# Performance work log

Hardware: AMD Instinct MI355X
Metric: run time of the kernel (lower is better)

The kernel has to match this reference:

```python
import jax, jax.numpy as jnp
import numpy as np

MASK_VALUE = -1e30


def setup_inputs() -> dict:
    key = jax.random.key(0)
    ks = jax.random.split(key, 8)
    B, N, M, D = 64, 1024, 128, 256
    c = jax.random.normal(ks[0], (B, N, D), dtype=jnp.float32)
    q = jax.random.normal(ks[1], (B, M, D), dtype=jnp.float32)
    c_mask = jax.random.randint(ks[2], (B, N), 0, 2, dtype=jnp.int32)
    q_mask = jax.random.randint(ks[3], (B, M), 0, 2, dtype=jnp.int32)
    w0 = jax.random.normal(ks[4], (D, 1), dtype=jnp.float32) * 0.06  # glorot-ish scale
    w1 = jax.random.normal(ks[5], (D, 1), dtype=jnp.float32) * 0.06
    wm = jax.random.normal(ks[6], (D,), dtype=jnp.float32) * 0.06
    bias = jnp.zeros((M,), dtype=jnp.float32)
    return {"c": c, "q": q, "c_mask": c_mask, "q_mask": q_mask,
            "w0": w0, "w1": w1, "wm": wm, "bias": bias}


def reference(c, q, c_mask, q_mask, w0, w1, wm, bias):
    # Trilinear similarity S[b,i,j] = c.w0 + q.w1 + sum_d c*wm*q + bias[j]
    sub0 = jnp.einsum('bnd,do->bno', c, w0)              # (B,N,1)
    sub1 = jnp.einsum('bmd,do->bom', q, w1)              # (B,1,M)
    sub2 = jnp.einsum('bnd,d,bmd->bnm', c, wm, q)        # (B,N,M)
    S = sub0 + sub1 + sub2 + bias                        # bias broadcast over last axis
    qm = q_mask.astype(jnp.float32)[:, None, :]          # (B,1,M)
    cm = c_mask.astype(jnp.float32)[:, :, None]          # (B,N,1)
    S_ = jax.nn.softmax(S + MASK_VALUE * (1.0 - qm), axis=-1)   # row softmax over query
    S_T = jnp.swapaxes(jax.nn.softmax(S + MASK_VALUE * (1.0 - cm), axis=1), 1, 2)  # (B,M,N)
    c2q = jnp.matmul(S_, q)                              # (B,N,D)
    q2c = jnp.matmul(jnp.matmul(S_, S_T), c)             # (B,N,D)
    return jnp.concatenate([c, c2q, c * c2q, c * q2c], axis=-1)  # (B,N,4D)
```

## Files before the change

### kernel.cpp

```cpp
#include <hip/hip_runtime.h>
#include <cfloat>

#define BB 64
#define NN 1024
#define MM 128
#define DD 256
#define MASKV (-1e30f)

typedef __attribute__((ext_vector_type(8))) short bf16x8;
typedef __attribute__((ext_vector_type(16))) float f32x16;

__device__ __forceinline__ unsigned short f2bf(float x) {
  union { float f; unsigned int u; } v; v.f = x;
  unsigned int r = v.u + 0x7fffu + ((v.u >> 16) & 1u);
  return (unsigned short)(r >> 16);
}
__device__ __forceinline__ float bf2f(unsigned short h) {
  union { float f; unsigned int u; } v; v.u = ((unsigned int)h) << 16;
  return v.f;
}
__device__ __forceinline__ void split8(const float* xs, uint4* hv, uint4* lv) {
  unsigned hp[4], lp[4];
  #pragma unroll
  for (int p = 0; p < 4; p++) {
    unsigned short h0 = f2bf(xs[2 * p]), h1 = f2bf(xs[2 * p + 1]);
    unsigned short g0 = f2bf(xs[2 * p] - bf2f(h0));
    unsigned short g1 = f2bf(xs[2 * p + 1] - bf2f(h1));
    hp[p] = (unsigned)h0 | ((unsigned)h1 << 16);
    lp[p] = (unsigned)g0 | ((unsigned)g1 << 16);
  }
  *hv = make_uint4(hp[0], hp[1], hp[2], hp[3]);
  *lv = make_uint4(lp[0], lp[1], lp[2], lp[3]);
}
__device__ __forceinline__ bf16x8 u2b(uint4 u) {
  union { uint4 a; bf16x8 b; } x; x.a = u; return x.b;
}

__global__ __launch_bounds__(256) void k_dots(
    const float* __restrict__ c, const float* __restrict__ q,
    const int* __restrict__ qmask,
    const float* __restrict__ w0, const float* __restrict__ w1,
    const float* __restrict__ bias,
    float* __restrict__ sub0, float* __restrict__ qtermM) {
  int wave = (blockIdx.x * blockDim.x + threadIdx.x) >> 6;
  int lane = threadIdx.x & 63;
  const int total = BB * NN + BB * MM;
  if (wave >= total) return;
  const float* row;
  const float* w;
  if (wave < BB * NN) { row = c + (size_t)wave * DD; w = w0; }
  else                { row = q + (size_t)(wave - BB * NN) * DD; w = w1; }
  float4 v  = *(const float4*)(row + lane * 4);
  float4 wv = *(const float4*)(w   + lane * 4);
  float s = v.x * wv.x + v.y * wv.y + v.z * wv.z + v.w * wv.w;
  #pragma unroll
  for (int off = 32; off > 0; off >>= 1) s += __shfl_xor(s, off, 64);
  if (lane == 0) {
    if (wave < BB * NN) {
      sub0[wave] = s;
    } else {
      int r = wave - BB * NN;
      int m = r & (MM - 1);
      qtermM[r] = s + bias[m] + (qmask[r] ? 0.0f : MASKV);
    }
  }
}

__global__ __launch_bounds__(256) void k_zero(float* __restrict__ p) {
  p[blockIdx.x * 256 + threadIdx.x] = 0.0f;
}

__global__ __launch_bounds__(256) void k_pack_q(
    const float* __restrict__ q,
    unsigned short* __restrict__ dsth, unsigned short* __restrict__ dstl) {
  const int b = blockIdx.y;
  const int u = blockIdx.x * 4 + (threadIdx.x >> 6);
  const int f = u >> 3, ks = u & 7;
  const int l = threadIdx.x & 63;
  const int l31 = l & 31, lh = l >> 5;
  const float* sb = q + (size_t)b * MM * DD + (size_t)(ks * 16 + lh * 8) * DD + f * 32 + l31;
  float ys[8];
  #pragma unroll
  for (int j = 0; j < 8; j++) ys[j] = sb[(size_t)j * DD];
  uint4 hv, lv;
  split8(ys, &hv, &lv);
  size_t off = (size_t)b * 32768 + (size_t)(u * 64 + l) * 8;
  *(uint4*)(dsth + off) = hv;
  *(uint4*)(dstl + off) = lv;
}

__global__ __launch_bounds__(256) void k_pack_a(
    const float* __restrict__ Apart, const float* __restrict__ colsum,
    unsigned short* __restrict__ dsth, unsigned short* __restrict__ dstl) {
  const int b = blockIdx.y;
  const int u = blockIdx.x * 4 + (threadIdx.x >> 6);
  const int f = u >> 3, ks = u & 7;
  const int l = threadIdx.x & 63;
  const int l31 = l & 31, lh = l >> 5;
  const int m0 = ks * 16 + lh * 8;
  const size_t P = (size_t)BB * MM * DD;
  const float* sb = Apart + (size_t)b * MM * DD + (size_t)m0 * DD + f * 32 + l31;
  float ys[8];
  #pragma unroll
  for (int j = 0; j < 8; j++) {
    float v = sb[(size_t)j * DD] + sb[P + (size_t)j * DD] +
              sb[2 * P + (size_t)j * DD] + sb[3 * P + (size_t)j * DD];
    ys[j] = v * (1.0f / colsum[b * MM + m0 + j]);
  }
  uint4 hv, lv;
  split8(ys, &hv, &lv);
  size_t off = (size_t)b * 32768 + (size_t)(u * 64 + l) * 8;
  *(uint4*)(dsth + off) = hv;
  *(uint4*)(dstl + off) = lv;
}

__global__ __launch_bounds__(256) void k_score(
    const float* __restrict__ c, const float* __restrict__ q,
    const int* __restrict__ cmask, const float* __restrict__ wm,
    const float* __restrict__ sub0, const float* __restrict__ qtermM,
    unsigned short* __restrict__ Sfh, unsigned short* __restrict__ Sfl,
    unsigned short* __restrict__ EThi, unsigned short* __restrict__ ETlo,
    float* __restrict__ colsum) {
  __shared__ unsigned short smem[32768];
  unsigned short* cwh = smem;
  unsigned short* cwl = smem + 8192;
  unsigned short* qhi = smem + 16384;
  unsigned short* qlo = smem + 24576;
  const int b = blockIdx.y;
  const int n0 = blockIdx.x * 128;
  const int t = threadIdx.x;
  const int w = t >> 6;
  const int l = t & 63;
  const int l31 = l & 31;
  const int lh = l >> 5;

  f32x16 acc[4];
  #pragma unroll
  for (int mb = 0; mb < 4; mb++)
    #pragma unroll
    for (int i = 0; i < 16; i++) acc[mb][i] = 0.0f;

  for (int k0 = 0; k0 < DD; k0 += 64) {
    __syncthreads();
    #pragma unroll
    for (int g = 0; g < 4; g++) {
      int lin = t + g * 256;
      int row = lin >> 3;
      int kg  = (lin & 7) * 8;
      unsigned boff = (unsigned)(row * 128 + ((kg * 2) ^ ((row & 7) << 4)));
      float4 w0v = *(const float4*)(wm + k0 + kg);
      float4 w1v = *(const float4*)(wm + k0 + kg + 4);
      const float* cp = c + (size_t)(b * NN + n0 + row) * DD + k0 + kg;
      float4 a0 = *(const float4*)cp;
      float4 a1 = *(const float4*)(cp + 4);
      float xs[8] = {a0.x * w0v.x, a0.y * w0v.y, a0.z * w0v.z, a0.w * w0v.w,
                     a1.x * w1v.x, a1.y * w1v.y, a1.z * w1v.z, a1.w * w1v.w};
      uint4 hv, lv;
      split8(xs, &hv, &lv);
      *(uint4*)((char*)cwh + boff) = hv;
      *(uint4*)((char*)cwl + boff) = lv;
      const float* qp = q + (size_t)(b * MM + row) * DD + k0 + kg;
      float4 b0 = *(const float4*)qp;
      float4 b1 = *(const float4*)(qp + 4);
      float ys[8] = {b0.x, b0.y, b0.z, b0.w, b1.x, b1.y, b1.z, b1.w};
      split8(ys, &hv, &lv);
      *(uint4*)((char*)qhi + boff) = hv;
      *(uint4*)((char*)qlo + boff) = lv;
    }
    __syncthreads();
    #pragma unroll
    for (int ks = 0; ks < 64; ks += 16) {
      int ak = ks + lh * 8;
      unsigned arow = (unsigned)(w * 32 + l31);
      unsigned aoff = arow * 128 + (((unsigned)(ak * 2)) ^ ((arow & 7) << 4));
      bf16x8 ah = *(const bf16x8*)((const char*)cwh + aoff);
      bf16x8 al = *(const bf16x8*)((const char*)cwl + aoff);
      #pragma unroll
      for (int mb = 0; mb < 4; mb++) {
        unsigned brow = (unsigned)(mb * 32 + l31);
        unsigned boff2 = brow * 128 + (((unsigned)(ak * 2)) ^ ((brow & 7) << 4));
        bf16x8 bh = *(const bf16x8*)((const char*)qhi + boff2);
        bf16x8 bl = *(const bf16x8*)((const char*)qlo + boff2);
        acc[mb] = __builtin_amdgcn_mfma_f32_32x32x16_bf16(ah, bh, acc[mb], 0, 0, 0);
        acc[mb] = __builtin_amdgcn_mfma_f32_32x32x16_bf16(ah, bl, acc[mb], 0, 0, 0);
        acc[mb] = __builtin_amdgcn_mfma_f32_32x32x16_bf16(al, bh, acc[mb], 0, 0, 0);
      }
    }
  }

  unsigned* stile = (unsigned*)smem;
  unsigned short* eth = smem;
  unsigned short* etl = smem + 16384;
  __syncthreads();

  float qt[4];
  #pragma unroll
  for (int mb = 0; mb < 4; mb++) qt[mb] = qtermM[b * MM + mb * 32 + l31];

  float s0m[16];
  float ps[4] = {0.f, 0.f, 0.f, 0.f};
  #pragma unroll
  for (int g = 0; g < 4; g++) {
    #pragma unroll
    for (int j = 0; j < 4; j++) {
      int r = 4 * g + j;
      int row = j + 8 * g + 4 * lh;
      int gn = n0 + w * 32 + row;
      float sv = sub0[b * NN + gn] + (cmask[b * NN + gn] ? 0.0f : MASKV);
      s0m[g * 4 + j] = sv;
      float x[4];
      float vmax = -FLT_MAX;
      #pragma unroll
      for (int mb = 0; mb < 4; mb++) { x[mb] = acc[mb][r] + qt[mb]; vmax = fmaxf(vmax, x[mb]); }
      #pragma unroll
      for (int off = 16; off > 0; off >>= 1) vmax = fmaxf(vmax, __shfl_xor(vmax, off, 64));
      float e[4];
      float vsum = 0.0f;
      #pragma unroll
      for (int mb = 0; mb < 4; mb++) { e[mb] = __expf(x[mb] - vmax); vsum += e[mb]; }
      #pragma unroll
      for (int off = 16; off > 0; off >>= 1) vsum += __shfl_xor(vsum, off, 64);
      float inv = 1.0f / vsum;
      int nloc = w * 32 + 8 * g + 4 * lh + j;
      unsigned swn = (unsigned)((nloc & 15) << 4);
      #pragma unroll
      for (int mb = 0; mb < 4; mb++) {
        float s = e[mb] * inv;
        unsigned short h = f2bf(s);
        unsigned short lo2 = f2bf(s - bf2f(h));
        unsigned v = (unsigned)h | ((unsigned)lo2 << 16);
        int m = mb * 32 + l31;
        *(unsigned*)((char*)stile + nloc * 512 + (((unsigned)(m * 4)) ^ swn)) = v;
        float Ev = __expf(acc[mb][r] + sv);
        ps[mb] += Ev;
      }
    }
  }
  #pragma unroll
  for (int mb = 0; mb < 4; mb++) {
    ps[mb] += __shfl_xor(ps[mb], 32, 64);
    if (lh == 0) atomicAdd(&colsum[b * MM + mb * 32 + l31], ps[mb]);
  }
  __syncthreads();

  {
    size_t tb = ((size_t)b * 32 + (size_t)blockIdx.x * 4 + w) * 4096;
    int nloc = w * 32 + l31;
    unsigned basen = (unsigned)(nloc * 512);
    unsigned swn = (unsigned)((nloc & 15) << 4);
    #pragma unroll
    for (int ks = 0; ks < 8; ks++) {
      unsigned mB = (unsigned)((lh * 8 + ks * 16) * 4);
      uint4 va = *(const uint4*)((const char*)stile + basen + (mB ^ swn));
      uint4 vb = *(const uint4*)((const char*)stile + basen + ((mB + 16) ^ swn));
      uint4 hv = make_uint4((va.x & 0xFFFFu) | (va.y << 16), (va.z & 0xFFFFu) | (va.w << 16),
                            (vb.x & 0xFFFFu) | (vb.y << 16), (vb.z & 0xFFFFu) | (vb.w << 16));
      uint4 lv = make_uint4((va.x >> 16) | (va.y & 0xFFFF0000u), (va.z >> 16) | (va.w & 0xFFFF0000u),
                            (vb.x >> 16) | (vb.y & 0xFFFF0000u), (vb.z >> 16) | (vb.w & 0xFFFF0000u));
      size_t off = tb + (size_t)(ks * 64 + l) * 8;
      *(uint4*)(Sfh + off) = hv;
      *(uint4*)(Sfl + off) = lv;
    }
  }
  __syncthreads();

  #pragma unroll
  for (int g = 0; g < 4; g++) {
    float evg[4][4];
    #pragma unroll
    for (int j = 0; j < 4; j++) {
      int r = 4 * g + j;
      #pragma unroll
      for (int mb = 0; mb < 4; mb++)
        evg[mb][j] = __expf(acc[mb][r] + s0m[g * 4 + j]);
    }
    int nloc = w * 32 + 8 * g + 4 * lh;
    #pragma unroll
    for (int mb = 0; mb < 4; mb++) {
      int m = mb * 32 + l31;
      unsigned short h[4], lo[4];
      #pragma unroll
      for (int j = 0; j < 4; j++) {
        h[j] = f2bf(evg[mb][j]);
        lo[j] = f2bf(evg[mb][j] - bf2f(h[j]));
      }
      unsigned addr = (unsigned)(m * 256 + ((nloc * 2) ^ ((m & 15) << 4)));
      *(uint2*)((char*)eth + addr) = make_uint2(
          (unsigned)h[0] | ((unsigned)h[1] << 16),
          (unsigned)h[2] | ((unsigned)h[3] << 16));
      *(uint2*)((char*)etl + addr) = make_uint2(
          (unsigned)lo[0] | ((unsigned)lo[1] << 16),
          (unsigned)lo[2] | ((unsigned)lo[3] << 16));
    }
  }
  __syncthreads();

  {
    int chunk = t & 15;
    int mrow0 = t >> 4;
    #pragma unroll
    for (int it = 0; it < 8; it++) {
      int m = it * 16 + mrow0;
      int sw = (chunk * 16) ^ ((m & 15) << 4);
      uint4 vh = *(const uint4*)((const char*)eth + m * 256 + sw);
      uint4 vl = *(const uint4*)((const char*)etl + m * 256 + sw);
      size_t gb = (size_t)(b * MM + m) * NN + n0 + chunk * 8;
      *(uint4*)(EThi + gb) = vh;
      *(uint4*)(ETlo + gb) = vl;
    }
  }
}

__global__ __launch_bounds__(512) void k_colA(
    const unsigned short* __restrict__ EThi, const unsigned short* __restrict__ ETlo,
    const float* __restrict__ c, float* __restrict__ Apart) {
  const int p = blockIdx.x;
  const int b = blockIdx.y;
  const int t = threadIdx.x;
  const int w = t >> 6;
  const int l = t & 63;
  const int l31 = l & 31, lh = l >> 5;
  const int d = w * 32 + l31;

  f32x16 acc[4];
  #pragma unroll
  for (int mf = 0; mf < 4; mf++)
    #pragma unroll
    for (int i = 0; i < 16; i++) acc[mf][i] = 0.0f;

  const float* cb = c + (size_t)b * NN * DD + d;
  const size_t etb = (size_t)b * MM * NN + (size_t)p * 256 + lh * 8;

  for (int ks = 0; ks < 16; ks++) {
    int nb = p * 256 + ks * 16 + lh * 8;
    float ys[8];
    #pragma unroll
    for (int j = 0; j < 8; j++) ys[j] = cb[(size_t)(nb + j) * DD];
    uint4 hv, lv;
    split8(ys, &hv, &lv);
    bf16x8 ah = u2b(hv), al = u2b(lv);
    #pragma unroll
    for (int mf = 0; mf < 4; mf++) {
      size_t eoff = etb + (size_t)(mf * 32 + l31) * NN + ks * 16;
      bf16x8 bh = *(const bf16x8*)(EThi + eoff);
      bf16x8 bl = *(const bf16x8*)(ETlo + eoff);
      acc[mf] = __builtin_amdgcn_mfma_f32_32x32x16_bf16(ah, bh, acc[mf], 0, 0, 0);
      acc[mf] = __builtin_amdgcn_mfma_f32_32x32x16_bf16(ah, bl, acc[mf], 0, 0, 0);
      acc[mf] = __builtin_amdgcn_mfma_f32_32x32x16_bf16(al, bh, acc[mf], 0, 0, 0);
    }
  }

  float* ap = Apart + (size_t)p * (BB * MM * DD);
  #pragma unroll
  for (int mf = 0; mf < 4; mf++) {
    size_t rowb = (size_t)(b * MM + mf * 32 + l31) * DD + w * 32 + 4 * lh;
    #pragma unroll
    for (int g = 0; g < 4; g++) {
      float4 o = make_float4(acc[mf][4 * g + 0], acc[mf][4 * g + 1],
                             acc[mf][4 * g + 2], acc[mf][4 * g + 3]);
      *(float4*)(ap + rowb + 8 * g) = o;
    }
  }
}

__global__ __launch_bounds__(512, 4) void k_out(
    const float* __restrict__ c,
    const unsigned short* __restrict__ Sfh, const unsigned short* __restrict__ Sfl,
    const unsigned short* __restrict__ qfh, const unsigned short* __restrict__ qfl,
    const unsigned short* __restrict__ afh, const unsigned short* __restrict__ afl,
    float* __restrict__ out) {
  const int b = blockIdx.y;
  const int n0 = blockIdx.x * 32;
  const int t = threadIdx.x;
  const int w = t >> 6;
  const int l = t & 63;
  const int l31 = l & 31;
  const int lh = l >> 5;

  f32x16 acc0, acc1;
  #pragma unroll
  for (int i = 0; i < 16; i++) { acc0[i] = 0.0f; acc1[i] = 0.0f; }

  const size_t so = ((size_t)b * 32 + blockIdx.x) * 4096 + (size_t)l * 8;
  const size_t fo = (size_t)b * 32768 + (size_t)(w * 8 * 64 + l) * 8;

  #pragma unroll
  for (int ks = 0; ks < 8; ks++) {
    bf16x8 ah = *(const bf16x8*)(Sfh + so + ks * 512);
    bf16x8 al = *(const bf16x8*)(Sfl + so + ks * 512);
    size_t off = fo + (size_t)(ks * 64) * 8;
    bf16x8 qh = *(const bf16x8*)(qfh + off);
    bf16x8 ql = *(const bf16x8*)(qfl + off);
    bf16x8 vh = *(const bf16x8*)(afh + off);
    bf16x8 vl = *(const bf16x8*)(afl + off);
    acc0 = __builtin_amdgcn_mfma_f32_32x32x16_bf16(ah, qh, acc0, 0, 0, 0);
    acc0 = __builtin_amdgcn_mfma_f32_32x32x16_bf16(ah, ql, acc0, 0, 0, 0);
    acc0 = __builtin_amdgcn_mfma_f32_32x32x16_bf16(al, qh, acc0, 0, 0, 0);
    acc1 = __builtin_amdgcn_mfma_f32_32x32x16_bf16(ah, vh, acc1, 0, 0, 0);
    acc1 = __builtin_amdgcn_mfma_f32_32x32x16_bf16(ah, vl, acc1, 0, 0, 0);
    acc1 = __builtin_amdgcn_mfma_f32_32x32x16_bf16(al, vh, acc1, 0, 0, 0);
  }

  const int d = w * 32 + l31;
  #pragma unroll
  for (int r = 0; r < 16; r++) {
    int row = (r & 3) + 8 * (r >> 2) + 4 * lh;
    int gn = n0 + row;
    float cv = c[(size_t)(b * NN + gn) * DD + d];
    size_t ob = (size_t)(b * NN + gn) * (4 * DD) + d;
    float v1 = acc0[r], v3 = acc1[r];
    out[ob]          = cv;
    out[ob + DD]     = v1;
    out[ob + 2 * DD] = cv * v1;
    out[ob + 3 * DD] = cv * v3;
  }
}

extern "C" void kernel_launch(void* const* d_in, const int* in_sizes, int n_in,
                              void* d_out, int out_size, void* d_ws, size_t ws_size,
                              hipStream_t stream) {
  const float* c     = (const float*)d_in[0];
  const float* q     = (const float*)d_in[1];
  const int*   cmask = (const int*)d_in[2];
  const int*   qmask = (const int*)d_in[3];
  const float* w0    = (const float*)d_in[4];
  const float* w1    = (const float*)d_in[5];
  const float* wm    = (const float*)d_in[6];
  const float* bias  = (const float*)d_in[7];
  float* out = (float*)d_out;
  float* ws  = (float*)d_ws;

  unsigned short* Sfh  = (unsigned short*)ws;
  unsigned short* Sfl  = Sfh + 8388608;
  unsigned short* EThi = (unsigned short*)(ws + 8388608);
  unsigned short* ETlo = (unsigned short*)(ws + 12582912);
  float* Apart  = ws + 16777216;
  unsigned short* qfh = (unsigned short*)(ws + 25165824);
  unsigned short* qfl = (unsigned short*)(ws + 26214400);
  unsigned short* afh = (unsigned short*)(ws + 27262976);
  unsigned short* afl = (unsigned short*)(ws + 28311552);
  float* sub0   = ws + 29360128;
  float* qtermM = ws + 29425664;
  float* colsum = ws + 29433856;

  k_dots<<<18432, 256, 0, stream>>>(c, q, qmask, w0, w1, bias, sub0, qtermM);
  k_zero<<<32, 256, 0, stream>>>(colsum);
  k_pack_q<<<dim3(16, BB), 256, 0, stream>>>(q, qfh, qfl);
  k_score<<<dim3(8, BB), 256, 0, stream>>>(c, q, cmask, wm, sub0, qtermM, Sfh, Sfl, EThi, ETlo, colsum);
  k_colA<<<dim3(4, BB), 512, 0, stream>>>(EThi, ETlo, c, Apart);
  k_pack_a<<<dim3(16, BB), 256, 0, stream>>>(Apart, colsum, afh, afl);
  k_out<<<dim3(32, BB), 512, 0, stream>>>(c, Sfh, Sfl, qfh, qfl, afh, afl, out);
}
```

Before: 487.7 us.

## Fuse row dot products into score kernel and split colA over more partitions

Removes the separate k_dots and k_zero kernels. The c·w0 and q·w1 dot products are now computed inside k_score's tile-load loop, reduced with shuffles and staged through shared memory. Colsum zeroing moves into k_pack_q. k_colA now splits N into 8 partitions instead of 4, which doubles the grid for more parallelism, and k_pack_a sums 8 partial buffers in exchange. The cost is a larger Apart workspace, more partial-sum traffic, and redundant q·w1 work in each score block.

```diff
diff --git a/kernel.cpp b/kernel.cpp
--- a/kernel.cpp
+++ b/kernel.cpp
@@ -36,44 +36,12 @@
   union { uint4 a; bf16x8 b; } x; x.a = u; return x.b;
 }
 
-__global__ __launch_bounds__(256) void k_dots(
-    const float* __restrict__ c, const float* __restrict__ q,
-    const int* __restrict__ qmask,
-    const float* __restrict__ w0, const float* __restrict__ w1,
-    const float* __restrict__ bias,
-    float* __restrict__ sub0, float* __restrict__ qtermM) {
-  int wave = (blockIdx.x * blockDim.x + threadIdx.x) >> 6;
-  int lane = threadIdx.x & 63;
-  const int total = BB * NN + BB * MM;
-  if (wave >= total) return;
-  const float* row;
-  const float* w;
-  if (wave < BB * NN) { row = c + (size_t)wave * DD; w = w0; }
-  else                { row = q + (size_t)(wave - BB * NN) * DD; w = w1; }
-  float4 v  = *(const float4*)(row + lane * 4);
-  float4 wv = *(const float4*)(w   + lane * 4);
-  float s = v.x * wv.x + v.y * wv.y + v.z * wv.z + v.w * wv.w;
-  #pragma unroll
-  for (int off = 32; off > 0; off >>= 1) s += __shfl_xor(s, off, 64);
-  if (lane == 0) {
-    if (wave < BB * NN) {
-      sub0[wave] = s;
-    } else {
-      int r = wave - BB * NN;
-      int m = r & (MM - 1);
-      qtermM[r] = s + bias[m] + (qmask[r] ? 0.0f : MASKV);
-    }
-  }
-}
-
-__global__ __launch_bounds__(256) void k_zero(float* __restrict__ p) {
-  p[blockIdx.x * 256 + threadIdx.x] = 0.0f;
-}
-
 __global__ __launch_bounds__(256) void k_pack_q(
     const float* __restrict__ q,
-    unsigned short* __restrict__ dsth, unsigned short* __restrict__ dstl) {
+    unsigned short* __restrict__ dsth, unsigned short* __restrict__ dstl,
+    float* __restrict__ colsum) {
   const int b = blockIdx.y;
+  if (blockIdx.x == 0 && threadIdx.x < MM) colsum[b * MM + threadIdx.x] = 0.0f;
   const int u = blockIdx.x * 4 + (threadIdx.x >> 6);
   const int f = u >> 3, ks = u & 7;
   const int l = threadIdx.x & 63;
@@ -103,8 +71,9 @@
   float ys[8];
   #pragma unroll
   for (int j = 0; j < 8; j++) {
-    float v = sb[(size_t)j * DD] + sb[P + (size_t)j * DD] +
-              sb[2 * P + (size_t)j * DD] + sb[3 * P + (size_t)j * DD];
+    float v = 0.0f;
+    #pragma unroll
+    for (int p = 0; p < 8; p++) v += sb[(size_t)p * P + (size_t)j * DD];
     ys[j] = v * (1.0f / colsum[b * MM + m0 + j]);
   }
   uint4 hv, lv;
@@ -116,8 +85,10 @@
 
 __global__ __launch_bounds__(256) void k_score(
     const float* __restrict__ c, const float* __restrict__ q,
-    const int* __restrict__ cmask, const float* __restrict__ wm,
-    const float* __restrict__ sub0, const float* __restrict__ qtermM,
+    const int* __restrict__ cmask, const int* __restrict__ qmask,
+    const float* __restrict__ wm,
+    const float* __restrict__ w0, const float* __restrict__ w1,
+    const float* __restrict__ bias,
     unsigned short* __restrict__ Sfh, unsigned short* __restrict__ Sfl,
     unsigned short* __restrict__ EThi, unsigned short* __restrict__ ETlo,
     float* __restrict__ colsum) {
@@ -140,6 +111,9 @@
     #pragma unroll
     for (int i = 0; i < 16; i++) acc[mb][i] = 0.0f;
 
+  float csum[4] = {0.f, 0.f, 0.f, 0.f};
+  float qsum[4] = {0.f, 0.f, 0.f, 0.f};
+
   for (int k0 = 0; k0 < DD; k0 += 64) {
     __syncthreads();
     #pragma unroll
@@ -148,13 +122,19 @@
       int row = lin >> 3;
       int kg  = (lin & 7) * 8;
       unsigned boff = (unsigned)(row * 128 + ((kg * 2) ^ ((row & 7) << 4)));
-      float4 w0v = *(const float4*)(wm + k0 + kg);
-      float4 w1v = *(const float4*)(wm + k0 + kg + 4);
+      float4 wma = *(const float4*)(wm + k0 + kg);
+      float4 wmb = *(const float4*)(wm + k0 + kg + 4);
+      float4 w0a = *(const float4*)(w0 + k0 + kg);
+      float4 w0b = *(const float4*)(w0 + k0 + kg + 4);
+      float4 w1a = *(const float4*)(w1 + k0 + kg);
+      float4 w1b = *(const float4*)(w1 + k0 + kg + 4);
       const float* cp = c + (size_t)(b * NN + n0 + row) * DD + k0 + kg;
       float4 a0 = *(const float4*)cp;
       float4 a1 = *(const float4*)(cp + 4);
-      float xs[8] = {a0.x * w0v.x, a0.y * w0v.y, a0.z * w0v.z, a0.w * w0v.w,
-                     a1.x * w1v.x, a1.y * w1v.y, a1.z * w1v.z, a1.w * w1v.w};
+      csum[g] += a0.x * w0a.x + a0.y * w0a.y + a0.z * w0a.z + a0.w * w0a.w +
+                 a1.x * w0b.x + a1.y * w0b.y + a1.z * w0b.z + a1.w * w0b.w;
+      float xs[8] = {a0.x * wma.x, a0.y * wma.y, a0.z * wma.z, a0.w * wma.w,
+                     a1.x * wmb.x, a1.y * wmb.y, a1.z * wmb.z, a1.w * wmb.w};
       uint4 hv, lv;
       split8(xs, &hv, &lv);
       *(uint4*)((char*)cwh + boff) = hv;
@@ -162,6 +142,8 @@
       const float* qp = q + (size_t)(b * MM + row) * DD + k0 + kg;
       float4 b0 = *(const float4*)qp;
       float4 b1 = *(const float4*)(qp + 4);
+      qsum[g] += b0.x * w1a.x + b0.y * w1a.y + b0.z * w1a.z + b0.w * w1a.w +
+                 b1.x * w1b.x + b1.y * w1b.y + b1.z * w1b.z + b1.w * w1b.w;
       float ys[8] = {b0.x, b0.y, b0.z, b0.w, b1.x, b1.y, b1.z, b1.w};
       split8(ys, &hv, &lv);
       *(uint4*)((char*)qhi + boff) = hv;
@@ -188,26 +170,49 @@
     }
   }
 
+  __syncthreads();
+  float* s0_l = (float*)smem;
+  float* qt_l = (float*)smem + 128;
+  #pragma unroll
+  for (int g = 0; g < 4; g++) {
+    #pragma unroll
+    for (int off = 1; off < 8; off <<= 1) {
+      csum[g] += __shfl_xor(csum[g], off, 64);
+      qsum[g] += __shfl_xor(qsum[g], off, 64);
+    }
+  }
+  if ((t & 7) == 0) {
+    #pragma unroll
+    for (int g = 0; g < 4; g++) {
+      int row = (t + g * 256) >> 3;
+      s0_l[row] = csum[g] + (cmask[b * NN + n0 + row] ? 0.0f : MASKV);
+      qt_l[row] = qsum[g] + bias[row] + (qmask[b * MM + row] ? 0.0f : MASKV);
+    }
+  }
+  __syncthreads();
+
+  float qt[4];
+  #pragma unroll
+  for (int mb = 0; mb < 4; mb++) qt[mb] = qt_l[mb * 32 + l31];
+  float s0m[16];
+  #pragma unroll
+  for (int g = 0; g < 4; g++)
+    #pragma unroll
+    for (int j = 0; j < 4; j++)
+      s0m[g * 4 + j] = s0_l[w * 32 + j + 8 * g + 4 * lh];
+  __syncthreads();
+
   unsigned* stile = (unsigned*)smem;
   unsigned short* eth = smem;
   unsigned short* etl = smem + 16384;
-  __syncthreads();
-
-  float qt[4];
-  #pragma unroll
-  for (int mb = 0; mb < 4; mb++) qt[mb] = qtermM[b * MM + mb * 32 + l31];
-
-  float s0m[16];
+
   float ps[4] = {0.f, 0.f, 0.f, 0.f};
   #pragma unroll
   for (int g = 0; g < 4; g++) {
     #pragma unroll
     for (int j = 0; j < 4; j++) {
       int r = 4 * g + j;
-      int row = j + 8 * g + 4 * lh;
-      int gn = n0 + w * 32 + row;
-      float sv = sub0[b * NN + gn] + (cmask[b * NN + gn] ? 0.0f : MASKV);
-      s0m[g * 4 + j] = sv;
+      float sv = s0m[g * 4 + j];
       float x[4];
       float vmax = -FLT_MAX;
       #pragma unroll
@@ -329,10 +334,10 @@
     for (int i = 0; i < 16; i++) acc[mf][i] = 0.0f;
 
   const float* cb = c + (size_t)b * NN * DD + d;
-  const size_t etb = (size_t)b * MM * NN + (size_t)p * 256 + lh * 8;
-
-  for (int ks = 0; ks < 16; ks++) {
-    int nb = p * 256 + ks * 16 + lh * 8;
+  const size_t etb = (size_t)b * MM * NN + (size_t)p * 128 + lh * 8;
+
+  for (int ks = 0; ks < 8; ks++) {
+    int nb = p * 128 + ks * 16 + lh * 8;
     float ys[8];
     #pragma unroll
     for (int j = 0; j < 8; j++) ys[j] = cb[(size_t)(nb + j) * DD];
@@ -435,19 +440,16 @@
   unsigned short* EThi = (unsigned short*)(ws + 8388608);
   unsigned short* ETlo = (unsigned short*)(ws + 12582912);
   float* Apart  = ws + 16777216;
-  unsigned short* qfh = (unsigned short*)(ws + 25165824);
-  unsigned short* qfl = (unsigned short*)(ws + 26214400);
-  unsigned short* afh = (unsigned short*)(ws + 27262976);
-  unsigned short* afl = (unsigned short*)(ws + 28311552);
-  float* sub0   = ws + 29360128;
-  float* qtermM = ws + 29425664;
-  float* colsum = ws + 29433856;
-
-  k_dots<<<18432, 256, 0, stream>>>(c, q, qmask, w0, w1, bias, sub0, qtermM);
-  k_zero<<<32, 256, 0, stream>>>(colsum);
-  k_pack_q<<<dim3(16, BB), 256, 0, stream>>>(q, qfh, qfl);
-  k_score<<<dim3(8, BB), 256, 0, stream>>>(c, q, cmask, wm, sub0, qtermM, Sfh, Sfl, EThi, ETlo, colsum);
-  k_colA<<<dim3(4, BB), 512, 0, stream>>>(EThi, ETlo, c, Apart);
+  unsigned short* qfh = (unsigned short*)(ws + 33554432);
+  unsigned short* qfl = (unsigned short*)(ws + 34603008);
+  unsigned short* afh = (unsigned short*)(ws + 35651584);
+  unsigned short* afl = (unsigned short*)(ws + 36700160);
+  float* colsum = ws + 37748736;
+
+  k_pack_q<<<dim3(16, BB), 256, 0, stream>>>(q, qfh, qfl, colsum);
+  k_score<<<dim3(8, BB), 256, 0, stream>>>(c, q, cmask, qmask, wm, w0, w1, bias,
+                                           Sfh, Sfl, EThi, ETlo, colsum);
+  k_colA<<<dim3(8, BB), 512, 0, stream>>>(EThi, ETlo, c, Apart);
   k_pack_a<<<dim3(16, BB), 256, 0, stream>>>(Apart, colsum, afh, afl);
   k_out<<<dim3(32, BB), 512, 0, stream>>>(c, Sfh, Sfl, qfh, qfl, afh, afl, out);
 }
```

Result: slower. 510.5 us (+4.7%).
